# Performance work log

Hardware: AMD Instinct MI355X
Metric: run time of the kernel (lower is better)

Reference implementation:

```python
import jax, jax.numpy as jnp
import numpy as np

# Model dims (see init_kwargs / shape_source)
B = 2048      # batch
CIN = 256     # tabular input features (c_in)
NH = 512      # TabularEncoder hidden width
NENC_HID = 4  # nlayers=6 -> input layer + 4 hidden + output layer
NF = 112      # n_features = num_concepts (conv=False path)
K = 112       # num_concepts
NL = 50       # num_latent_concepts
MC = 100      # num_monte_carlo
NOUT = 200    # num_output


def setup_inputs() -> dict:
    key = jax.random.key(0)
    ks = jax.random.split(key, 8)
    x = jax.random.normal(ks[0], (B, CIN), dtype=jnp.float32)
    enc_Win = jax.random.normal(ks[1], (CIN, NH), dtype=jnp.float32) * (1.0 / np.sqrt(CIN))
    enc_bin = jnp.zeros((NH,), jnp.float32)
    enc_Wh = jax.random.normal(ks[2], (NENC_HID, NH, NH), dtype=jnp.float32) * (1.0 / np.sqrt(NH))
    enc_bh = jnp.zeros((NENC_HID, NH), jnp.float32)
    enc_Wout = jax.random.normal(ks[3], (NH, NF), dtype=jnp.float32) * (1.0 / np.sqrt(NH))
    enc_bout = jnp.zeros((NF,), jnp.float32)
    # Per-concept predictor i has first Linear of shape [NF+i, NL]; pad all to [NF+K, NL]
    # and statically slice rows [:NF+i] in the loop (unused padded rows never touched).
    pred_W1 = jax.random.normal(ks[4], (K, NF + K, NL), dtype=jnp.float32) * (1.0 / np.sqrt(NF))
    pred_b1 = jnp.zeros((K, NL), jnp.float32)
    pred_W2 = jax.random.normal(ks[5], (K, NL), dtype=jnp.float32) * (1.0 / np.sqrt(NL))
    pred_b2 = jnp.zeros((K,), jnp.float32)
    head_W = jax.random.normal(ks[6], (K, NOUT), dtype=jnp.float32) * (1.0 / np.sqrt(K))
    head_b = jnp.zeros((NOUT,), jnp.float32)
    return {
        "x": x,
        "enc_Win": enc_Win, "enc_bin": enc_bin,
        "enc_Wh": enc_Wh, "enc_bh": enc_bh,
        "enc_Wout": enc_Wout, "enc_bout": enc_bout,
        "pred_W1": pred_W1, "pred_b1": pred_b1,
        "pred_W2": pred_W2, "pred_b2": pred_b2,
        "head_W": head_W, "head_b": head_b,
        "epoch": 0,
    }


def reference(x, enc_Win, enc_bin, enc_Wh, enc_bh, enc_Wout, enc_bout,
              pred_W1, pred_b1, pred_W2, pred_b2, head_W, head_b, epoch):
    lrelu = jax.nn.leaky_relu  # negative_slope=0.01, matches nn.LeakyReLU default

    # ---- TabularEncoder (ni=CIN, nhidden=NH, nlayers=6, no=NF) ----
    h = lrelu(x @ enc_Win + enc_bin)
    for i in range(enc_Wh.shape[0]):
        h = lrelu(h @ enc_Wh[i] + enc_bh[i])
    inter = h @ enc_Wout + enc_bout                      # [B, NF]
    Bn = inter.shape[0]

    key = jax.random.key(42)
    c_hard = jnp.zeros((Bn, K, MC), inter.dtype)
    c_probs = []
    for i in range(K):
        W1 = pred_W1[i, :NF + i]                          # [NF+i, NL]
        base = inter @ W1[:NF] + pred_b1[i]               # [B, NL], shared across MC
        if i == 0:
            p1 = jax.nn.sigmoid(lrelu(base) @ pred_W2[i] + pred_b2[i])   # [B]
            p = jnp.broadcast_to(p1[:, None], (Bn, MC))   # expand(-1,-1,MC)
        else:
            # add contribution of the i previously sampled hard concepts, per MC sample
            hpre = base[:, None, :] + jnp.einsum('bim,ih->bmh', c_hard[:, :i], W1[NF:])  # [B,MC,NL]
            p = jax.nn.sigmoid(jnp.einsum('bmh,h->bm', lrelu(hpre), pred_W2[i]) + pred_b2[i])  # [B,MC]
        key, sk = jax.random.split(key)
        samp = jax.random.bernoulli(sk, p).astype(p.dtype)  # torch.bernoulli(concept)
        c_hard = c_hard.at[:, i, :].set(samp)
        c_probs.append(p)

    c_prob = jnp.stack(c_probs, axis=1)                   # [B, K, MC]

    # ---- Head: MC average of softmax probabilities (pred_dim > 1 branch) ----
    logits = jnp.einsum('bkm,ko->bmo', c_hard, head_W) + head_b   # [B, MC, NOUT]
    probs = jax.nn.softmax(logits, axis=-1).mean(axis=1)          # [B, NOUT]
    y_pred_logits = jnp.log(probs + 1e-6)
    return (c_prob, y_pred_logits, c_hard)
```

## Files before the change

kernel.cpp:

```cpp
#include <hip/hip_runtime.h>

typedef unsigned int u32;
typedef unsigned short u16;
typedef unsigned long long u64;

#define YOFF  22937600ull
#define CHOFF 23347200ull

#define OFF_HA    0ull
#define OFF_HB    4194304ull
#define OFF_INTER 8388608ull

__host__ __device__ inline u32 rotl32_(u32 x, int r) { return (x << r) | (x >> (32 - r)); }
__host__ __device__ inline void tf2x32(u32 k0, u32 k1, u32 c0, u32 c1, u32& o0, u32& o1) {
  u32 ks0 = k0, ks1 = k1, ks2 = k0 ^ k1 ^ 0x1BD11BDAu;
  u32 x0 = c0 + ks0, x1 = c1 + ks1;
  const int RA[4] = {13, 15, 26, 6}, RB[4] = {17, 29, 16, 24};
  for (int i = 0; i < 5; ++i) {
    const int* R = (i & 1) ? RB : RA;
    for (int j = 0; j < 4; ++j) { x0 += x1; x1 = rotl32_(x1, R[j]); x1 ^= x0; }
    switch (i) {
      case 0: x0 += ks1; x1 += ks2 + 1u; break;
      case 1: x0 += ks2; x1 += ks0 + 2u; break;
      case 2: x0 += ks0; x1 += ks1 + 3u; break;
      case 3: x0 += ks1; x1 += ks2 + 4u; break;
      case 4: x0 += ks2; x1 += ks0 + 5u; break;
    }
  }
  o0 = x0; o1 = x1;
}

struct SKeys { u32 v[224]; };

template <bool DO_LRELU>
__global__ __launch_bounds__(256) void gemm_bias(const float* __restrict__ A,
                                                 const float* __restrict__ Bm,
                                                 const float* __restrict__ bias,
                                                 float* __restrict__ C,
                                                 int M, int N, int K) {
  __shared__ float As[32][33];
  __shared__ float Bs[32][65];
  const int bm = blockIdx.y * 32, bn = blockIdx.x * 64;
  const int t = threadIdx.x;
  const int ty = t >> 4, tx = t & 15;
  float acc[2][4] = {};
  for (int k0 = 0; k0 < K; k0 += 32) {
    {
      int e = t;
      int m = e >> 3, k4 = e & 7;
      float4 v = *(const float4*)(A + (size_t)(bm + m) * K + (k0 + k4 * 4));
      As[k4 * 4 + 0][m] = v.x; As[k4 * 4 + 1][m] = v.y;
      As[k4 * 4 + 2][m] = v.z; As[k4 * 4 + 3][m] = v.w;
    }
#pragma unroll
    for (int l = 0; l < 2; ++l) {
      int e = l * 256 + t;
      int k = e >> 4, n4 = e & 15;
      int gn = bn + n4 * 4;
      if (gn < N) {
        float4 v = *(const float4*)(Bm + (size_t)(k0 + k) * N + gn);
        Bs[k][n4 * 4 + 0] = v.x; Bs[k][n4 * 4 + 1] = v.y;
        Bs[k][n4 * 4 + 2] = v.z; Bs[k][n4 * 4 + 3] = v.w;
      } else {
        Bs[k][n4 * 4 + 0] = 0.f; Bs[k][n4 * 4 + 1] = 0.f;
        Bs[k][n4 * 4 + 2] = 0.f; Bs[k][n4 * 4 + 3] = 0.f;
      }
    }
    __syncthreads();
#pragma unroll
    for (int kk = 0; kk < 32; ++kk) {
      float a[2], b[4];
#pragma unroll
      for (int j = 0; j < 2; ++j) a[j] = As[kk][ty * 2 + j];
#pragma unroll
      for (int j = 0; j < 4; ++j) b[j] = Bs[kk][tx * 4 + j];
#pragma unroll
      for (int i = 0; i < 2; ++i)
#pragma unroll
        for (int j = 0; j < 4; ++j) acc[i][j] = fmaf(a[i], b[j], acc[i][j]);
    }
    __syncthreads();
  }
#pragma unroll
  for (int i = 0; i < 2; ++i) {
#pragma unroll
    for (int j = 0; j < 4; ++j) {
      int m = bm + ty * 2 + i, n = bn + tx * 4 + j;
      if (n < N) {
        float s = acc[i][j] + bias[n];
        if (DO_LRELU) { if (s < 0.f) s = 0.01f * s; }
        C[(size_t)m * N + n] = s;
      }
    }
  }
}

__global__ __launch_bounds__(256) void base_kernel(const float* __restrict__ inter,
                                                   const float* __restrict__ W1,
                                                   const float* __restrict__ pb1,
                                                   float* __restrict__ out) {
  __shared__ float As[112][65];
  __shared__ float Ws[112][64];
  const int i = blockIdx.y;
  const int b0 = blockIdx.x * 64;
  const int t = threadIdx.x;
  const int ty = t >> 4, tx = t & 15;
#pragma unroll
  for (int l = 0; l < 7; ++l) {
    int e4 = l * 256 + t;
    int k4 = e4 % 28, bs = e4 / 28;
    float4 v = *(const float4*)(inter + (size_t)(b0 + bs) * 112 + k4 * 4);
    As[k4 * 4 + 0][bs] = v.x; As[k4 * 4 + 1][bs] = v.y;
    As[k4 * 4 + 2][bs] = v.z; As[k4 * 4 + 3][bs] = v.w;
  }
#pragma unroll
  for (int l = 0; l < 28; ++l) {
    int e = l * 256 + t;
    int r = e >> 6, c = e & 63;
    Ws[r][c] = (c < 50) ? W1[(size_t)i * 11200 + r * 50 + c] : 0.f;
  }
  __syncthreads();
  float acc[4][4] = {};
  for (int kk = 0; kk < 112; ++kk) {
    float a[4], b[4];
#pragma unroll
    for (int j = 0; j < 4; ++j) { a[j] = As[kk][ty * 4 + j]; b[j] = Ws[kk][tx * 4 + j]; }
#pragma unroll
    for (int ii = 0; ii < 4; ++ii)
#pragma unroll
      for (int j = 0; j < 4; ++j) acc[ii][j] = fmaf(a[ii], b[j], acc[ii][j]);
  }
#pragma unroll
  for (int ii = 0; ii < 4; ++ii) {
#pragma unroll
    for (int j = 0; j < 4; ++j) {
      int b = b0 + ty * 4 + ii, h = tx * 4 + j;
      if (h < 50) {
        out[CHOFF + (size_t)b * 11200 + (size_t)i * 100 + h] = acc[ii][j] + pb1[i * 50 + h];
      }
    }
  }
}

__global__ __launch_bounds__(256) void sample_kernel6(const float* __restrict__ W1,
                                                      const float* __restrict__ W2,
                                                      const float* __restrict__ b2v,
                                                      float* __restrict__ out,
                                                      u32* __restrict__ masks, SKeys sks) {
  const int t = threadIdx.x;
  const int p = blockIdx.x * 256 + t;
  const int b = p / 100;
  const int m = p - b * 100;
  const float* __restrict__ baserow = out + CHOFF + (size_t)b * 11200;
  u64 lo = 0, hi = 0;

  for (int i = 0; i < 112; ++i) {
    const float* __restrict__ Wi = W1 + (size_t)i * 11200 + 5600;
    float acc[50];
#pragma unroll
    for (int h = 0; h < 50; ++h) acc[h] = 0.f;
    {
      int r = 0;
      int r1 = (i < 64) ? i : 64;
      u64 cm = lo;
#pragma unroll 2
      for (; r < r1; ++r) {
        float c = (cm & 1ull) ? 1.f : 0.f;
        cm >>= 1;
        const float* __restrict__ wrA = Wi + r * 50;
        const float* __restrict__ wrB = wrA + 25;
#pragma unroll
        for (int h = 0; h < 25; ++h) acc[h] = fmaf(c, wrA[h], acc[h]);
#pragma unroll
        for (int h = 0; h < 25; ++h) acc[25 + h] = fmaf(c, wrB[h], acc[25 + h]);
      }
      cm = hi;
#pragma unroll 2
      for (; r < i; ++r) {
        float c = (cm & 1ull) ? 1.f : 0.f;
        cm >>= 1;
        const float* __restrict__ wrA = Wi + r * 50;
        const float* __restrict__ wrB = wrA + 25;
#pragma unroll
        for (int h = 0; h < 25; ++h) acc[h] = fmaf(c, wrA[h], acc[h]);
#pragma unroll
        for (int h = 0; h < 25; ++h) acc[25 + h] = fmaf(c, wrB[h], acc[25 + h]);
      }
    }
    const float* __restrict__ w2 = W2 + i * 50;
    const float* bs = baserow + (size_t)i * 100;
    float s = 0.f;
#pragma unroll
    for (int h = 0; h < 50; ++h) {
      float v = acc[h] + bs[h];
      if (v < 0.f) v = 0.01f * v;
      s = fmaf(v, w2[h], s);
    }
    float l = s + b2v[i];
    float pr = 1.f / (1.f + expf(-l));
    u32 a0, a1;
    tf2x32(sks.v[2 * i], sks.v[2 * i + 1], 0u, (u32)p, a0, a1);
    u32 fb = ((a0 ^ a1) >> 9) | 0x3F800000u;
    float uu; __builtin_memcpy(&uu, &fb, 4); uu -= 1.f;
    u64 sbit = (uu < pr) ? 1ull : 0ull;
    out[(size_t)b * 11200 + (size_t)i * 100 + m] = pr;
    if (i < 64) lo |= sbit << i; else hi |= sbit << (i - 64);
  }
  u32* mp = masks + (size_t)p * 4;
  mp[0] = (u32)lo; mp[1] = (u32)(lo >> 32);
  mp[2] = (u32)hi; mp[3] = (u32)(hi >> 32);
}

__global__ __launch_bounds__(256) void expand_kernel(const u32* __restrict__ masks,
                                                     float* __restrict__ out) {
  __shared__ u32 mW[100][4];
  const int b = blockIdx.x;
  const int t = threadIdx.x;
  if (t < 100) {
    const u32* mp = masks + ((size_t)b * 100 + t) * 4;
    mW[t][0] = mp[0]; mW[t][1] = mp[1]; mW[t][2] = mp[2]; mW[t][3] = mp[3];
  }
  __syncthreads();
  for (int e = t; e < 11200; e += 256) {
    int i = e / 100, m = e - i * 100;
    u32 word = mW[m][i >> 5];
    out[CHOFF + (size_t)b * 11200 + e] = (float)((word >> (i & 31)) & 1u);
  }
}

__global__ __launch_bounds__(256) void head_kernel(const float* __restrict__ HW,
                                                   const float* __restrict__ hb,
                                                   float* __restrict__ out) {
  __shared__ unsigned char cS[100][116];
  __shared__ float lgS[50][201];
  const int b = blockIdx.x;
  const int t = threadIdx.x;
  for (int e = t; e < 11200; e += 256) {
    int k = e / 100, m = e - k * 100;
    cS[m][k] = (out[CHOFF + (size_t)b * 11200 + (size_t)k * 100 + m] != 0.f) ? 1 : 0;
  }
  __syncthreads();
  float pacc = 0.f;
  for (int mh = 0; mh < 2; ++mh) {
    for (int l = 0; l < 3; ++l) {
      int tile = l * 256 + t;
      if (tile < 625) {
        int o0 = (tile % 25) * 8;
        int m0 = (tile / 25) * 2;
        float acc[2][8] = {};
        for (int k = 0; k < 112; ++k) {
          float4 wa = *(const float4*)(HW + (size_t)k * 200 + o0);
          float4 wb = *(const float4*)(HW + (size_t)k * 200 + o0 + 4);
          float w[8] = {wa.x, wa.y, wa.z, wa.w, wb.x, wb.y, wb.z, wb.w};
          float c0 = (float)cS[mh * 50 + m0][k];
          float c1 = (float)cS[mh * 50 + m0 + 1][k];
#pragma unroll
          for (int jo = 0; jo < 8; ++jo) {
            acc[0][jo] = fmaf(c0, w[jo], acc[0][jo]);
            acc[1][jo] = fmaf(c1, w[jo], acc[1][jo]);
          }
        }
#pragma unroll
        for (int im = 0; im < 2; ++im)
#pragma unroll
          for (int jo = 0; jo < 8; ++jo) {
            int o = o0 + jo;
            lgS[m0 + im][o] = acc[im][jo] + hb[o];
          }
      }
    }
    __syncthreads();
    if (t < 50) {
      int m = t;
      float mx = -3.0e38f;
      for (int o = 0; o < 200; ++o) mx = fmaxf(mx, lgS[m][o]);
      float s = 0.f;
      for (int o = 0; o < 200; ++o) {
        float e = expf(lgS[m][o] - mx);
        lgS[m][o] = e; s += e;
      }
      float inv = 1.f / s;
      for (int o = 0; o < 200; ++o) lgS[m][o] = lgS[m][o] * inv;
    }
    __syncthreads();
    if (t < 200) { for (int m = 0; m < 50; ++m) pacc += lgS[m][t]; }
    __syncthreads();
  }
  if (t < 200) {
    out[YOFF + (size_t)b * 200 + t] = logf(pacc / 100.f + 1e-6f);
  }
}

extern "C" void kernel_launch(void* const* d_in, const int* in_sizes, int n_in,
                              void* d_out, int out_size, void* d_ws, size_t ws_size,
                              hipStream_t stream) {
  const float* x    = (const float*)d_in[0];
  const float* Win  = (const float*)d_in[1];
  const float* bin  = (const float*)d_in[2];
  const float* Wh   = (const float*)d_in[3];
  const float* bh   = (const float*)d_in[4];
  const float* Wout = (const float*)d_in[5];
  const float* bout = (const float*)d_in[6];
  const float* pW1  = (const float*)d_in[7];
  const float* pb1  = (const float*)d_in[8];
  const float* pW2  = (const float*)d_in[9];
  const float* pb2  = (const float*)d_in[10];
  const float* hW   = (const float*)d_in[11];
  const float* hb   = (const float*)d_in[12];
  float* out = (float*)d_out;
  char* ws = (char*)d_ws;

  float* hA     = (float*)(ws + OFF_HA);
  float* hB     = (float*)(ws + OFF_HB);
  float* interB = (float*)(ws + OFF_INTER);
  u32*   masks  = (u32*)(ws + OFF_HB);

  gemm_bias<true ><<<dim3(8, 64), 256, 0, stream>>>(x,  Win,             bin,          hA,     2048, 512, 256);
  gemm_bias<true ><<<dim3(8, 64), 256, 0, stream>>>(hA, Wh + 0 * 262144, bh + 0 * 512, hB,     2048, 512, 512);
  gemm_bias<true ><<<dim3(8, 64), 256, 0, stream>>>(hB, Wh + 1 * 262144, bh + 1 * 512, hA,     2048, 512, 512);
  gemm_bias<true ><<<dim3(8, 64), 256, 0, stream>>>(hA, Wh + 2 * 262144, bh + 2 * 512, hB,     2048, 512, 512);
  gemm_bias<true ><<<dim3(8, 64), 256, 0, stream>>>(hB, Wh + 3 * 262144, bh + 3 * 512, hA,     2048, 512, 512);
  gemm_bias<false><<<dim3(2, 64), 256, 0, stream>>>(hA, Wout,            bout,         interB, 2048, 112, 512);

  base_kernel<<<dim3(32, 112), 256, 0, stream>>>(interB, pW1, pb1, out);

  SKeys sks;
  {
    u32 k0 = 0u, k1 = 42u;
    for (int i = 0; i < 112; ++i) {
      u32 nk0, nk1, s0, s1;
      tf2x32(k0, k1, 0u, 0u, nk0, nk1);
      tf2x32(k0, k1, 0u, 1u, s0, s1);
      sks.v[2 * i] = s0; sks.v[2 * i + 1] = s1;
      k0 = nk0; k1 = nk1;
    }
  }
  sample_kernel6<<<800, 256, 0, stream>>>(pW1, pW2, pb2, out, masks, sks);
  expand_kernel<<<2048, 256, 0, stream>>>(masks, out);

  head_kernel<<<2048, 256, 0, stream>>>(hW, hb, out);
}
```

Measured before the change: 3.652 ms.

## Restructure sequential sampling as per-batch block with register-tiled MC×hidden work split

Replaces the one-thread-per-(batch,MC) sampler, which held 50 accumulators per thread and streamed the W1 rows per thread, with one block per batch row. Each thread computes a 4×5 tile of MC samples × hidden units, and the sampled concept bits are shared through shared-memory ballot masks. The expand kernel is folded into the same kernel's epilogue. Each of the 112 steps now needs two block-wide barriers, only 100 threads do the reduction and sampling phase, and 6 threads per block sit idle during accumulation.

```diff
diff --git a/kernel.cpp b/kernel.cpp
--- a/kernel.cpp
+++ b/kernel.cpp
@@ -142,89 +142,91 @@
   }
 }
 
-__global__ __launch_bounds__(256) void sample_kernel6(const float* __restrict__ W1,
+__global__ __launch_bounds__(256, 4) void sample_gemm(const float* __restrict__ W1,
                                                       const float* __restrict__ W2,
                                                       const float* __restrict__ b2v,
-                                                      float* __restrict__ out,
-                                                      u32* __restrict__ masks, SKeys sks) {
+                                                      float* __restrict__ out, SKeys sks) {
+  __shared__ float vacc[100][51];
+  __shared__ u32 cm[112][4];
   const int t = threadIdx.x;
-  const int p = blockIdx.x * 256 + t;
-  const int b = p / 100;
-  const int m = p - b * 100;
-  const float* __restrict__ baserow = out + CHOFF + (size_t)b * 11200;
-  u64 lo = 0, hi = 0;
+  const int b = blockIdx.x;
+  const float* __restrict__ stage = out + CHOFF + (size_t)b * 11200;
+
+  const int mg = t / 10;
+  const int hg = t - mg * 10;
+  const int m0 = mg * 4;
+  const int h0 = hg * 5;
+  const int cword = mg >> 3;
+  const int cshift = (mg * 4) & 31;
 
   for (int i = 0; i < 112; ++i) {
-    const float* __restrict__ Wi = W1 + (size_t)i * 11200 + 5600;
-    float acc[50];
-#pragma unroll
-    for (int h = 0; h < 50; ++h) acc[h] = 0.f;
-    {
-      int r = 0;
-      int r1 = (i < 64) ? i : 64;
-      u64 cm = lo;
-#pragma unroll 2
-      for (; r < r1; ++r) {
-        float c = (cm & 1ull) ? 1.f : 0.f;
-        cm >>= 1;
-        const float* __restrict__ wrA = Wi + r * 50;
-        const float* __restrict__ wrB = wrA + 25;
-#pragma unroll
-        for (int h = 0; h < 25; ++h) acc[h] = fmaf(c, wrA[h], acc[h]);
-#pragma unroll
-        for (int h = 0; h < 25; ++h) acc[25 + h] = fmaf(c, wrB[h], acc[25 + h]);
-      }
-      cm = hi;
-#pragma unroll 2
-      for (; r < i; ++r) {
-        float c = (cm & 1ull) ? 1.f : 0.f;
-        cm >>= 1;
-        const float* __restrict__ wrA = Wi + r * 50;
-        const float* __restrict__ wrB = wrA + 25;
-#pragma unroll
-        for (int h = 0; h < 25; ++h) acc[h] = fmaf(c, wrA[h], acc[h]);
-#pragma unroll
-        for (int h = 0; h < 25; ++h) acc[25 + h] = fmaf(c, wrB[h], acc[25 + h]);
-      }
-    }
-    const float* __restrict__ w2 = W2 + i * 50;
-    const float* bs = baserow + (size_t)i * 100;
-    float s = 0.f;
-#pragma unroll
-    for (int h = 0; h < 50; ++h) {
-      float v = acc[h] + bs[h];
-      if (v < 0.f) v = 0.01f * v;
-      s = fmaf(v, w2[h], s);
-    }
-    float l = s + b2v[i];
-    float pr = 1.f / (1.f + expf(-l));
-    u32 a0, a1;
-    tf2x32(sks.v[2 * i], sks.v[2 * i + 1], 0u, (u32)p, a0, a1);
-    u32 fb = ((a0 ^ a1) >> 9) | 0x3F800000u;
-    float uu; __builtin_memcpy(&uu, &fb, 4); uu -= 1.f;
-    u64 sbit = (uu < pr) ? 1ull : 0ull;
-    out[(size_t)b * 11200 + (size_t)i * 100 + m] = pr;
-    if (i < 64) lo |= sbit << i; else hi |= sbit << (i - 64);
-  }
-  u32* mp = masks + (size_t)p * 4;
-  mp[0] = (u32)lo; mp[1] = (u32)(lo >> 32);
-  mp[2] = (u32)hi; mp[3] = (u32)(hi >> 32);
-}
-
-__global__ __launch_bounds__(256) void expand_kernel(const u32* __restrict__ masks,
-                                                     float* __restrict__ out) {
-  __shared__ u32 mW[100][4];
-  const int b = blockIdx.x;
-  const int t = threadIdx.x;
-  if (t < 100) {
-    const u32* mp = masks + ((size_t)b * 100 + t) * 4;
-    mW[t][0] = mp[0]; mW[t][1] = mp[1]; mW[t][2] = mp[2]; mW[t][3] = mp[3];
-  }
-  __syncthreads();
+    if (t < 250) {
+      float acc[4][5];
+#pragma unroll
+      for (int mi = 0; mi < 4; ++mi)
+#pragma unroll
+        for (int hi = 0; hi < 5; ++hi) acc[mi][hi] = 0.f;
+      const float* __restrict__ Wi = W1 + (size_t)i * 11200 + 5600 + h0;
+      for (int r = 0; r < i; ++r) {
+        u32 win = cm[r][cword] >> cshift;
+        float c0 = (float)(win & 1u);
+        float c1 = (float)((win >> 1) & 1u);
+        float c2 = (float)((win >> 2) & 1u);
+        float c3 = (float)((win >> 3) & 1u);
+        const float* __restrict__ wr = Wi + r * 50;
+        float w0 = wr[0], w1 = wr[1], w2c = wr[2], w3 = wr[3], w4 = wr[4];
+        acc[0][0] = fmaf(c0, w0, acc[0][0]); acc[0][1] = fmaf(c0, w1, acc[0][1]);
+        acc[0][2] = fmaf(c0, w2c, acc[0][2]); acc[0][3] = fmaf(c0, w3, acc[0][3]);
+        acc[0][4] = fmaf(c0, w4, acc[0][4]);
+        acc[1][0] = fmaf(c1, w0, acc[1][0]); acc[1][1] = fmaf(c1, w1, acc[1][1]);
+        acc[1][2] = fmaf(c1, w2c, acc[1][2]); acc[1][3] = fmaf(c1, w3, acc[1][3]);
+        acc[1][4] = fmaf(c1, w4, acc[1][4]);
+        acc[2][0] = fmaf(c2, w0, acc[2][0]); acc[2][1] = fmaf(c2, w1, acc[2][1]);
+        acc[2][2] = fmaf(c2, w2c, acc[2][2]); acc[2][3] = fmaf(c2, w3, acc[2][3]);
+        acc[2][4] = fmaf(c2, w4, acc[2][4]);
+        acc[3][0] = fmaf(c3, w0, acc[3][0]); acc[3][1] = fmaf(c3, w1, acc[3][1]);
+        acc[3][2] = fmaf(c3, w2c, acc[3][2]); acc[3][3] = fmaf(c3, w3, acc[3][3]);
+        acc[3][4] = fmaf(c3, w4, acc[3][4]);
+      }
+      const float* __restrict__ bsrc = stage + (size_t)i * 100 + h0;
+      float bsv[5];
+#pragma unroll
+      for (int hi = 0; hi < 5; ++hi) bsv[hi] = bsrc[hi];
+#pragma unroll
+      for (int mi = 0; mi < 4; ++mi)
+#pragma unroll
+        for (int hi = 0; hi < 5; ++hi) {
+          float v = acc[mi][hi] + bsv[hi];
+          if (v < 0.f) v = 0.01f * v;
+          vacc[m0 + mi][h0 + hi] = v;
+        }
+    }
+    __syncthreads();
+    if (t < 100) {
+      const int m = t;
+      const float* __restrict__ w2 = W2 + i * 50;
+      float s = 0.f;
+#pragma unroll
+      for (int h = 0; h < 50; ++h) s = fmaf(vacc[m][h], w2[h], s);
+      float l = s + b2v[i];
+      float pr = 1.f / (1.f + expf(-l));
+      const int p = b * 100 + m;
+      u32 a0, a1;
+      tf2x32(sks.v[2 * i], sks.v[2 * i + 1], 0u, (u32)p, a0, a1);
+      u32 fb = ((a0 ^ a1) >> 9) | 0x3F800000u;
+      float uu; __builtin_memcpy(&uu, &fb, 4); uu -= 1.f;
+      int smp = (uu < pr) ? 1 : 0;
+      out[(size_t)b * 11200 + (size_t)i * 100 + m] = pr;
+      u64 bal = __ballot(smp);
+      if (t == 0)  { cm[i][0] = (u32)bal; cm[i][1] = (u32)(bal >> 32); }
+      if (t == 64) { cm[i][2] = (u32)bal; cm[i][3] = (u32)(bal >> 32); }
+    }
+    __syncthreads();
+  }
   for (int e = t; e < 11200; e += 256) {
     int i = e / 100, m = e - i * 100;
-    u32 word = mW[m][i >> 5];
-    out[CHOFF + (size_t)b * 11200 + e] = (float)((word >> (i & 31)) & 1u);
+    u32 bit = (cm[i][m >> 5] >> (m & 31)) & 1u;
+    out[CHOFF + (size_t)b * 11200 + e] = (float)bit;
   }
 }
 
@@ -313,7 +315,6 @@
   float* hA     = (float*)(ws + OFF_HA);
   float* hB     = (float*)(ws + OFF_HB);
   float* interB = (float*)(ws + OFF_INTER);
-  u32*   masks  = (u32*)(ws + OFF_HB);
 
   gemm_bias<true ><<<dim3(8, 64), 256, 0, stream>>>(x,  Win,             bin,          hA,     2048, 512, 256);
   gemm_bias<true ><<<dim3(8, 64), 256, 0, stream>>>(hA, Wh + 0 * 262144, bh + 0 * 512, hB,     2048, 512, 512);
@@ -335,8 +336,7 @@
       k0 = nk0; k1 = nk1;
     }
   }
-  sample_kernel6<<<800, 256, 0, stream>>>(pW1, pW2, pb2, out, masks, sks);
-  expand_kernel<<<2048, 256, 0, stream>>>(masks, out);
+  sample_gemm<<<2048, 256, 0, stream>>>(pW1, pW2, pb2, out, sks);
 
   head_kernel<<<2048, 256, 0, stream>>>(hW, hb, out);
 }
```

New measurement: 5.996 ms. 1.64x slower.
